# Performance work log

Measured on AMD Instinct MI355X. Metric: run time of the kernel, lower is better.

Reference implementation:

```python
import jax, jax.numpy as jnp
import numpy as np

D_MODEL = 1024
N_HEADS = 16
D_HEAD = D_MODEL // N_HEADS
D_FF = 4096
EPS = 1e-5


def layer_norm(x, g, b):
    mu = jnp.mean(x, axis=-1, keepdims=True)
    var = jnp.mean(jnp.square(x - mu), axis=-1, keepdims=True)
    return (x - mu) * jax.lax.rsqrt(var + EPS) * g + b


def setup_inputs() -> dict:
    key = jax.random.key(0)
    ks = jax.random.split(key, 8)
    s = 1.0 / np.sqrt(D_MODEL)
    return {
        "x": jax.random.normal(ks[0], (2, 2048, D_MODEL), dtype=jnp.float32),
        "Wq": jax.random.normal(ks[1], (N_HEADS, D_MODEL, D_HEAD), dtype=jnp.float32) * s,
        "Wk": jax.random.normal(ks[2], (N_HEADS, D_MODEL, D_HEAD), dtype=jnp.float32) * s,
        "Wv": jax.random.normal(ks[3], (N_HEADS, D_MODEL, D_HEAD), dtype=jnp.float32) * s,
        "Wo": jax.random.normal(ks[4], (D_MODEL, D_MODEL), dtype=jnp.float32) * s,
        "bo": jnp.zeros((D_MODEL,), dtype=jnp.float32),
        "ln1_g": jnp.ones((D_MODEL,), dtype=jnp.float32),
        "ln1_b": jnp.zeros((D_MODEL,), dtype=jnp.float32),
        "ln2_g": jnp.ones((D_MODEL,), dtype=jnp.float32),
        "ln2_b": jnp.zeros((D_MODEL,), dtype=jnp.float32),
        "W1": jax.random.normal(ks[5], (D_MODEL, D_FF), dtype=jnp.float32) * s,
        "b1": jnp.zeros((D_FF,), dtype=jnp.float32),
        "W2": jax.random.normal(ks[6], (D_FF, D_MODEL), dtype=jnp.float32) * (1.0 / np.sqrt(D_FF)),
        "b2": jnp.zeros((D_MODEL,), dtype=jnp.float32),
    }


def reference(x, Wq, Wk, Wv, Wo, bo, ln1_g, ln1_b, ln2_g, ln2_b, W1, b1, W2, b2):
    # Pre-norm MHA (per-head projections batched over head axis h)
    xn = layer_norm(x, ln1_g, ln1_b)
    q = jnp.einsum("bsd,hde->bhse", xn, Wq)
    k = jnp.einsum("bsd,hde->bhse", xn, Wk)
    v = jnp.einsum("bsd,hde->bhse", xn, Wv)
    scores = jnp.einsum("bhqe,bhke->bhqk", q, k) / jnp.sqrt(jnp.float32(D_HEAD))
    w = jax.nn.softmax(scores, axis=-1)
    attn = jnp.einsum("bhqk,bhke->bhqe", w, v)  # [b,h,s,dh]
    b, h, s, dh = attn.shape
    concat = attn.transpose(0, 2, 1, 3).reshape(b, s, h * dh)  # head concat order matches torch cat
    attn_out = concat @ Wo + bo
    hidden = x + attn_out
    hn = layer_norm(hidden, ln2_g, ln2_b)
    ff = jax.nn.gelu(hn @ W1 + b1, approximate=False) @ W2 + b2  # torch nn.GELU default = exact
    return hidden + ff
```

## Files before the change

kernel.cpp:

```cpp
#include <hip/hip_runtime.h>
#include <hip/hip_bf16.h>

typedef __bf16 bf16;
typedef __bf16 bf16x4 __attribute__((ext_vector_type(4)));
typedef __bf16 bf16x8 __attribute__((ext_vector_type(8)));
typedef float  f32x4  __attribute__((ext_vector_type(4)));

static __device__ __forceinline__ f32x4 mfma16(bf16x8 a, bf16x8 b, f32x4 c) {
  return __builtin_amdgcn_mfma_f32_16x16x32_bf16(a, b, c, 0, 0, 0);
}

static __device__ __forceinline__ void gl_lds16(const bf16* g, bf16* l) {
  __builtin_amdgcn_global_load_lds(
      (const __attribute__((address_space(1))) void*)g,
      (__attribute__((address_space(3))) void*)l, 16, 0, 0);
}

struct TrTab {
  const float* src[6];
  bf16* dst[6];
  int R[6], C[6], ntx[6], nty[6];
  int base[7];
};

__global__ __launch_bounds__(256) void tr6_kernel(TrTab tab) {
  int bid = blockIdx.x;
  int j = 0;
  while (j < 5 && bid >= tab.base[j + 1]) ++j;
  const int local = bid - tab.base[j];
  const int R = tab.R[j], C = tab.C[j];
  const int ntx = tab.ntx[j];
  const int per_z = ntx * tab.nty[j];
  const int z = local / per_z;
  const int rem = local - z * per_z;
  const int by = rem / ntx, bx = rem - by * ntx;
  const float* in = tab.src[j];
  bf16* out = tab.dst[j];

  __shared__ bf16 tile[32][33];
  const size_t zoff = (size_t)z * R * C;
  const int tx = threadIdx.x & 31, ty = threadIdx.x >> 5;
  const int x = bx * 32 + tx;
  const int y0 = by * 32;
#pragma unroll
  for (int jj = 0; jj < 4; ++jj)
    tile[ty + jj * 8][tx] = (bf16)in[zoff + (size_t)(y0 + ty + jj * 8) * C + x];
  __syncthreads();
  const int x2 = y0 + tx;
  const int y2 = bx * 32;
#pragma unroll
  for (int jj = 0; jj < 4; ++jj)
    out[zoff + (size_t)(y2 + ty + jj * 8) * R + x2] = tile[tx][ty + jj * 8];
}

__global__ __launch_bounds__(256) void trb_kernel(const bf16* __restrict__ inp,
                                                  bf16* __restrict__ out,
                                                  int R, int C) {
  __shared__ bf16 tile[32][33];
  const size_t zoff = (size_t)blockIdx.z * R * C;
  const int tx = threadIdx.x & 31, ty = threadIdx.x >> 5;
  const int x = blockIdx.x * 32 + tx;
  const int y0 = blockIdx.y * 32;
#pragma unroll
  for (int j = 0; j < 4; ++j)
    tile[ty + j * 8][tx] = inp[zoff + (size_t)(y0 + ty + j * 8) * C + x];
  __syncthreads();
  const int x2 = y0 + tx;
  const int y2 = blockIdx.x * 32;
#pragma unroll
  for (int j = 0; j < 4; ++j)
    out[zoff + (size_t)(y2 + ty + j * 8) * R + x2] = tile[tx][ty + j * 8];
}

__global__ __launch_bounds__(256) void ln_kernel(const float* __restrict__ inp,
                                                 const float* __restrict__ g,
                                                 const float* __restrict__ bt,
                                                 bf16* __restrict__ outp) {
  const int row = blockIdx.x;
  const int t = threadIdx.x;
  f32x4 v = ((const f32x4*)inp)[row * 256 + t];
  float s = v[0] + v[1] + v[2] + v[3];
  float sq = v[0] * v[0] + v[1] * v[1] + v[2] * v[2] + v[3] * v[3];
#pragma unroll
  for (int off = 32; off > 0; off >>= 1) {
    s += __shfl_xor(s, off);
    sq += __shfl_xor(sq, off);
  }
  __shared__ float red[8];
  const int wave = t >> 6, lane = t & 63;
  if (lane == 0) {
    red[wave] = s;
    red[wave + 4] = sq;
  }
  __syncthreads();
  s = red[0] + red[1] + red[2] + red[3];
  sq = red[4] + red[5] + red[6] + red[7];
  const float mu = s * (1.0f / 1024.0f);
  const float var = sq * (1.0f / 1024.0f) - mu * mu;
  const float rstd = rsqrtf(fmaxf(var, 0.0f) + 1e-5f);
  f32x4 gg = ((const f32x4*)g)[t];
  f32x4 bb = ((const f32x4*)bt)[t];
  bf16 o[4];
#pragma unroll
  for (int i = 0; i < 4; ++i)
    o[i] = (bf16)((v[i] - mu) * rstd * gg[i] + bb[i]);
  *(uint2*)&outp[(size_t)row * 1024 + 4 * t] = *(uint2*)o;
}

enum { EPI_QKV = 0, EPI_O = 1, EPI_FF1 = 2, EPI_FF2 = 3 };

template <int EPI, bool NARROW>
__global__ __launch_bounds__(256) void gemm_bt(
    const bf16* __restrict__ A, const bf16* __restrict__ Bt, const int K,
    const float* __restrict__ bias, const float* __restrict__ res,
    bf16* __restrict__ outB, float* __restrict__ outF) {
  constexpr int BN = NARROW ? 64 : 128;
  constexpr int NI = NARROW ? 2 : 4;
  __shared__ __align__(16) bf16 sA[128 * 64];
  __shared__ __align__(16) bf16 sB[BN * 64];
  const int t = threadIdx.x;
  const int lane = t & 63, wave = t >> 6;
  const int quad = lane >> 4, l15 = lane & 15;
  const int wr = wave >> 1, wc = wave & 1;
  const int m0 = blockIdx.y * 128, n0 = blockIdx.x * BN;
  const int srow = lane >> 3;
  const int scol = ((lane & 7) ^ srow) * 8;

  f32x4 acc[4][NI];
#pragma unroll
  for (int i = 0; i < 4; ++i)
#pragma unroll
    for (int j = 0; j < NI; ++j) acc[i][j] = {0.f, 0.f, 0.f, 0.f};

  for (int kt = 0; kt < K; kt += 64) {
    __syncthreads();
#pragma unroll
    for (int c = 0; c < 4; ++c) {
      const int chunk = wave * 4 + c;
      const int row = chunk * 8 + srow;
      gl_lds16(&A[(size_t)(m0 + row) * K + kt + scol], &sA[chunk * 512]);
    }
#pragma unroll
    for (int c = 0; c < BN / 32; ++c) {
      const int chunk = wave * (BN / 32) + c;
      const int row = chunk * 8 + srow;
      gl_lds16(&Bt[(size_t)(n0 + row) * K + kt + scol], &sB[chunk * 512]);
    }
    __syncthreads();
#pragma unroll
    for (int ks = 0; ks < 2; ++ks) {
      bf16x8 af[4], bfr[NI];
#pragma unroll
      for (int mi = 0; mi < 4; ++mi) {
        const int row = wr * 64 + mi * 16 + l15;
        const int col = ((ks * 4 + quad) ^ (row & 7)) * 8;
        af[mi] = *(const bf16x8*)&sA[row * 64 + col];
      }
#pragma unroll
      for (int ni = 0; ni < NI; ++ni) {
        const int row = wc * (BN / 2) + ni * 16 + l15;
        const int col = ((ks * 4 + quad) ^ (row & 7)) * 8;
        bfr[ni] = *(const bf16x8*)&sB[row * 64 + col];
      }
#pragma unroll
      for (int mi = 0; mi < 4; ++mi)
#pragma unroll
        for (int ni = 0; ni < NI; ++ni)
          acc[mi][ni] = mfma16(af[mi], bfr[ni], acc[mi][ni]);
    }
  }

#pragma unroll
  for (int mi = 0; mi < 4; ++mi) {
#pragma unroll
    for (int ni = 0; ni < NI; ++ni) {
      const int n = n0 + wc * (BN / 2) + ni * 16 + l15;
#pragma unroll
      for (int r = 0; r < 4; ++r) {
        const int m = m0 + wr * 64 + mi * 16 + quad * 4 + r;
        float v = acc[mi][ni][r];
        if constexpr (EPI == EPI_QKV) {
          const int which = n >> 10, nn = n & 1023;
          const int h = nn >> 6, e = nn & 63;
          const int b = m >> 11, s2 = m & 2047;
          outB[(size_t)which * 4194304 +
               ((size_t)(b * 16 + h) * 2048 + s2) * 64 + e] = (bf16)v;
        } else if constexpr (EPI == EPI_O) {
          v += bias[n] + res[(size_t)m * 1024 + n];
          outF[(size_t)m * 1024 + n] = v;
        } else if constexpr (EPI == EPI_FF1) {
          v += bias[n];
          v = 0.5f * v * (1.0f + erff(v * 0.70710678118654752f));
          outB[(size_t)m * 4096 + n] = (bf16)v;
        } else {
          v += bias[n] + res[(size_t)m * 1024 + n];
          outF[(size_t)m * 1024 + n] = v;
        }
      }
    }
  }
}

__global__ __launch_bounds__(256) void attn_kernel(const bf16* __restrict__ q,
                                                   const bf16* __restrict__ k,
                                                   const bf16* __restrict__ vt,
                                                   bf16* __restrict__ ao) {
  __shared__ __align__(16) bf16 sQP[64 * 72];
  __shared__ __align__(16) bf16 sK[64 * 64];
  __shared__ __align__(16) bf16 sV[64 * 64];
  const int t = threadIdx.x;
  const int lane = t & 63, wave = t >> 6;
  const int quad = lane >> 4, l15 = lane & 15;
  const int q0 = blockIdx.x * 64;
  const int bh = blockIdx.y;
  const int b = bh >> 4, h = bh & 15;
  const bf16* Q = q + (size_t)bh * 2048 * 64;
  const bf16* Kp = k + (size_t)bh * 2048 * 64;
  const bf16* Vt = vt + (size_t)bh * 64 * 2048;
  const int srow = lane >> 3;
  const int scol = ((lane & 7) ^ srow) * 8;
  const float SCL = 0.125f * 1.4426950408889634f;

#pragma unroll
  for (int c = 0; c < 2; ++c) {
    const int chunk = wave * 2 + c;
    const int row = chunk * 8 + srow;
    gl_lds16(&Q[(size_t)(q0 + row) * 64 + scol], &sQP[chunk * 512]);
  }
  __syncthreads();
  bf16x8 qf[2];
#pragma unroll
  for (int ks = 0; ks < 2; ++ks) {
    const int row = wave * 16 + l15;
    const int col = ((ks * 4 + quad) ^ (row & 7)) * 8;
    qf[ks] = *(const bf16x8*)&sQP[row * 64 + col];
  }

  f32x4 o[4];
  float lsum = 0.f;
#pragma unroll
  for (int ne = 0; ne < 4; ++ne) o[ne] = {0.f, 0.f, 0.f, 0.f};

  for (int kb = 0; kb < 32; ++kb) {
    const int kbase = kb * 64;
    __syncthreads();
#pragma unroll
    for (int c = 0; c < 2; ++c) {
      const int chunk = wave * 2 + c;
      const int row = chunk * 8 + srow;
      gl_lds16(&Kp[(size_t)(kbase + row) * 64 + scol], &sK[chunk * 512]);
      gl_lds16(&Vt[(size_t)row * 2048 + kbase + scol], &sV[chunk * 512]);
    }
    __syncthreads();

    f32x4 s[4];
#pragma unroll
    for (int ni = 0; ni < 4; ++ni) s[ni] = {0.f, 0.f, 0.f, 0.f};
#pragma unroll
    for (int ks = 0; ks < 2; ++ks) {
      bf16x8 kf[4];
#pragma unroll
      for (int ni = 0; ni < 4; ++ni) {
        const int row = ni * 16 + l15;
        const int col = ((ks * 4 + quad) ^ (row & 7)) * 8;
        kf[ni] = *(const bf16x8*)&sK[row * 64 + col];
      }
#pragma unroll
      for (int ni = 0; ni < 4; ++ni)
        s[ni] = mfma16(kf[ni], qf[ks], s[ni]);
    }

#pragma unroll
    for (int ni = 0; ni < 4; ++ni) {
      bf16x4 p4;
#pragma unroll
      for (int r = 0; r < 4; ++r) {
        const float p = exp2f(s[ni][r] * SCL);
        lsum += p;
        p4[r] = (bf16)p;
      }
      *(bf16x4*)&sQP[(wave * 16 + l15) * 72 + ni * 16 + quad * 4] = p4;
    }

#pragma unroll
    for (int ksb = 0; ksb < 2; ++ksb) {
      bf16x8 pf = *(const bf16x8*)&sQP[(wave * 16 + l15) * 72 +
                                       ksb * 32 + quad * 8];
      bf16x8 vf[4];
#pragma unroll
      for (int ne = 0; ne < 4; ++ne) {
        const int row = ne * 16 + l15;
        const int col = ((ksb * 4 + quad) ^ (row & 7)) * 8;
        vf[ne] = *(const bf16x8*)&sV[row * 64 + col];
      }
#pragma unroll
      for (int ne = 0; ne < 4; ++ne)
        o[ne] = mfma16(pf, vf[ne], o[ne]);
    }
  }

  lsum += __shfl_xor(lsum, 16);
  lsum += __shfl_xor(lsum, 32);
  const float linv_q = 1.0f / fmaxf(lsum, 1e-30f);
  float linv[4];
#pragma unroll
  for (int r = 0; r < 4; ++r)
    linv[r] = __shfl(linv_q, quad * 4 + r);
#pragma unroll
  for (int ne = 0; ne < 4; ++ne)
#pragma unroll
    for (int r = 0; r < 4; ++r) {
      const int row = q0 + wave * 16 + quad * 4 + r;
      const int col = h * 64 + ne * 16 + l15;
      ao[((size_t)(b * 2048 + row)) * 1024 + col] =
          (bf16)(o[ne][r] * linv[r]);
    }
}

extern "C" void kernel_launch(void* const* d_in, const int* in_sizes, int n_in,
                              void* d_out, int out_size, void* d_ws,
                              size_t ws_size, hipStream_t stream) {
  const float* x    = (const float*)d_in[0];
  const float* Wq   = (const float*)d_in[1];
  const float* Wk   = (const float*)d_in[2];
  const float* Wv   = (const float*)d_in[3];
  const float* Wo   = (const float*)d_in[4];
  const float* bo   = (const float*)d_in[5];
  const float* ln1g = (const float*)d_in[6];
  const float* ln1b = (const float*)d_in[7];
  const float* ln2g = (const float*)d_in[8];
  const float* ln2b = (const float*)d_in[9];
  const float* W1   = (const float*)d_in[10];
  const float* b1   = (const float*)d_in[11];
  const float* W2   = (const float*)d_in[12];
  const float* b2   = (const float*)d_in[13];

  char* ws = (char*)d_ws;
  const size_t MB = 1ull << 20;
  bf16* QKVT = (bf16*)(ws);
  bf16* WqT  = QKVT;
  bf16* WkT  = (bf16*)(ws + 2 * MB);
  bf16* WvT  = (bf16*)(ws + 4 * MB);
  bf16* WoT  = (bf16*)(ws + 6 * MB);
  bf16* W1T  = (bf16*)(ws + 8 * MB);
  bf16* W2T  = (bf16*)(ws + 16 * MB);
  bf16* sh8  = (bf16*)(ws + 24 * MB);
  bf16* qb   = (bf16*)(ws + 32 * MB);
  bf16* kb   = (bf16*)(ws + 40 * MB);
  bf16* vb   = (bf16*)(ws + 48 * MB);
  bf16* vtb  = (bf16*)(ws + 56 * MB);
  bf16* h1   = (bf16*)(ws + 32 * MB);
  float* hid = (float*)(ws + 64 * MB);

  const dim3 blk(256);

  TrTab tab;
  const float* srcs[6] = {Wq, Wk, Wv, Wo, W1, W2};
  bf16* dsts[6] = {WqT, WkT, WvT, WoT, W1T, W2T};
  const int Rs[6] = {1024, 1024, 1024, 1024, 1024, 4096};
  const int Cs[6] = {64, 64, 64, 1024, 4096, 1024};
  const int Zs[6] = {16, 16, 16, 1, 1, 1};
  int base = 0;
  for (int j = 0; j < 6; ++j) {
    tab.src[j] = srcs[j];
    tab.dst[j] = dsts[j];
    tab.R[j] = Rs[j];
    tab.C[j] = Cs[j];
    tab.ntx[j] = Cs[j] / 32;
    tab.nty[j] = Rs[j] / 32;
    tab.base[j] = base;
    base += (Cs[j] / 32) * (Rs[j] / 32) * Zs[j];
  }
  tab.base[6] = base;
  tr6_kernel<<<base, blk, 0, stream>>>(tab);

  ln_kernel<<<4096, blk, 0, stream>>>(x, ln1g, ln1b, sh8);
  gemm_bt<EPI_QKV, false><<<dim3(24, 32), blk, 0, stream>>>(
      sh8, QKVT, 1024, nullptr, nullptr, qb, nullptr);
  trb_kernel<<<dim3(2, 64, 32), blk, 0, stream>>>(vb, vtb, 2048, 64);
  attn_kernel<<<dim3(32, 32), blk, 0, stream>>>(qb, kb, vtb, sh8);
  gemm_bt<EPI_O, true><<<dim3(16, 32), blk, 0, stream>>>(
      sh8, WoT, 1024, bo, x, nullptr, hid);
  ln_kernel<<<4096, blk, 0, stream>>>(hid, ln2g, ln2b, sh8);
  gemm_bt<EPI_FF1, false><<<dim3(32, 32), blk, 0, stream>>>(
      sh8, W1T, 1024, b1, nullptr, h1, nullptr);
  gemm_bt<EPI_FF2, true><<<dim3(16, 32), blk, 0, stream>>>(
      h1, W2T, 4096, b2, hid, nullptr, (float*)d_out);

  (void)in_sizes; (void)n_in; (void)out_size; (void)ws_size;
}
```

Measured before the change: 378.2 us.

## Split attention keys across two wave groups with 128-query blocks and LDS merge

The attention kernel now uses 512-thread blocks covering 128 queries. Two groups of four waves each process half of the key sequence, and their output accumulators and row sums are merged through LDS at the end. Each wave now handles 32 query rows, so every K/V fragment read from LDS feeds two MFMAs, and the exp2 call switches to the hardware builtin. The cost is twice the register pressure per wave, an extra reduction step through shared memory, and half as many blocks in the grid.

```diff
diff --git a/kernel.cpp b/kernel.cpp
--- a/kernel.cpp
+++ b/kernel.cpp
@@ -8,6 +8,10 @@
 
 static __device__ __forceinline__ f32x4 mfma16(bf16x8 a, bf16x8 b, f32x4 c) {
   return __builtin_amdgcn_mfma_f32_16x16x32_bf16(a, b, c, 0, 0, 0);
+}
+
+static __device__ __forceinline__ float fexp2(float x) {
+  return __builtin_amdgcn_exp2f(x);
 }
 
 static __device__ __forceinline__ void gl_lds16(const bf16* g, bf16* l) {
@@ -201,22 +205,21 @@
   }
 }
 
-__global__ __launch_bounds__(256) void attn_kernel(const bf16* __restrict__ q,
-                                                   const bf16* __restrict__ k,
-                                                   const bf16* __restrict__ vt,
-                                                   bf16* __restrict__ ao) {
-  __shared__ __align__(16) bf16 sQP[64 * 72];
-  __shared__ __align__(16) bf16 sK[64 * 64];
-  __shared__ __align__(16) bf16 sV[64 * 64];
+__global__ __launch_bounds__(512, 4) void attn_kernel(
+    const bf16* __restrict__ q, const bf16* __restrict__ k,
+    const bf16* __restrict__ vt, bf16* __restrict__ ao) {
+  __shared__ __align__(16) bf16 sP[256 * 72];
+  __shared__ __align__(16) bf16 sK[2][64 * 64];
+  __shared__ __align__(16) bf16 sV[2][64 * 64];
   const int t = threadIdx.x;
   const int lane = t & 63, wave = t >> 6;
+  const int wq = wave & 3, kh = wave >> 2;
   const int quad = lane >> 4, l15 = lane & 15;
-  const int q0 = blockIdx.x * 64;
-  const int bh = blockIdx.y;
-  const int b = bh >> 4, h = bh & 15;
-  const bf16* Q = q + (size_t)bh * 2048 * 64;
-  const bf16* Kp = k + (size_t)bh * 2048 * 64;
-  const bf16* Vt = vt + (size_t)bh * 64 * 2048;
+  const int q0 = blockIdx.x * 128;
+  const int bh = blockIdx.y, b = bh >> 4, h = bh & 15;
+  const bf16* Q  = q  + (size_t)bh * 2048 * 64;
+  const bf16* Kp = k  + (size_t)bh * 2048 * 64 + (size_t)kh * 1024 * 64;
+  const bf16* Vt = vt + (size_t)bh * 64 * 2048 + kh * 1024;
   const int srow = lane >> 3;
   const int scol = ((lane & 7) ^ srow) * 8;
   const float SCL = 0.125f * 1.4426950408889634f;
@@ -225,37 +228,44 @@
   for (int c = 0; c < 2; ++c) {
     const int chunk = wave * 2 + c;
     const int row = chunk * 8 + srow;
-    gl_lds16(&Q[(size_t)(q0 + row) * 64 + scol], &sQP[chunk * 512]);
-  }
-  __syncthreads();
-  bf16x8 qf[2];
-#pragma unroll
-  for (int ks = 0; ks < 2; ++ks) {
-    const int row = wave * 16 + l15;
-    const int col = ((ks * 4 + quad) ^ (row & 7)) * 8;
-    qf[ks] = *(const bf16x8*)&sQP[row * 64 + col];
-  }
-
-  f32x4 o[4];
-  float lsum = 0.f;
-#pragma unroll
-  for (int ne = 0; ne < 4; ++ne) o[ne] = {0.f, 0.f, 0.f, 0.f};
-
-  for (int kb = 0; kb < 32; ++kb) {
+    gl_lds16(&Q[(size_t)(q0 + row) * 64 + scol], &sP[chunk * 512]);
+  }
+  __syncthreads();
+  bf16x8 qf[2][2];
+#pragma unroll
+  for (int mi = 0; mi < 2; ++mi)
+#pragma unroll
+    for (int ks = 0; ks < 2; ++ks) {
+      const int row = wq * 32 + mi * 16 + l15;
+      const int col = ((ks * 4 + quad) ^ (row & 7)) * 8;
+      qf[mi][ks] = *(const bf16x8*)&sP[row * 64 + col];
+    }
+  __syncthreads();
+
+  f32x4 o[2][4];
+  float ls[2] = {0.f, 0.f};
+#pragma unroll
+  for (int mi = 0; mi < 2; ++mi)
+#pragma unroll
+    for (int ne = 0; ne < 4; ++ne) o[mi][ne] = {0.f, 0.f, 0.f, 0.f};
+
+  for (int kb = 0; kb < 16; ++kb) {
     const int kbase = kb * 64;
     __syncthreads();
 #pragma unroll
     for (int c = 0; c < 2; ++c) {
-      const int chunk = wave * 2 + c;
+      const int chunk = wq * 2 + c;
       const int row = chunk * 8 + srow;
-      gl_lds16(&Kp[(size_t)(kbase + row) * 64 + scol], &sK[chunk * 512]);
-      gl_lds16(&Vt[(size_t)row * 2048 + kbase + scol], &sV[chunk * 512]);
+      gl_lds16(&Kp[(size_t)(kbase + row) * 64 + scol], &sK[kh][chunk * 512]);
+      gl_lds16(&Vt[(size_t)row * 2048 + kbase + scol], &sV[kh][chunk * 512]);
     }
     __syncthreads();
 
-    f32x4 s[4];
-#pragma unroll
-    for (int ni = 0; ni < 4; ++ni) s[ni] = {0.f, 0.f, 0.f, 0.f};
+    f32x4 s[4][2];
+#pragma unroll
+    for (int ni = 0; ni < 4; ++ni)
+#pragma unroll
+      for (int mi = 0; mi < 2; ++mi) s[ni][mi] = {0.f, 0.f, 0.f, 0.f};
 #pragma unroll
     for (int ks = 0; ks < 2; ++ks) {
       bf16x8 kf[4];
@@ -263,58 +273,99 @@
       for (int ni = 0; ni < 4; ++ni) {
         const int row = ni * 16 + l15;
         const int col = ((ks * 4 + quad) ^ (row & 7)) * 8;
-        kf[ni] = *(const bf16x8*)&sK[row * 64 + col];
+        kf[ni] = *(const bf16x8*)&sK[kh][row * 64 + col];
       }
 #pragma unroll
       for (int ni = 0; ni < 4; ++ni)
-        s[ni] = mfma16(kf[ni], qf[ks], s[ni]);
-    }
-
-#pragma unroll
-    for (int ni = 0; ni < 4; ++ni) {
-      bf16x4 p4;
-#pragma unroll
-      for (int r = 0; r < 4; ++r) {
-        const float p = exp2f(s[ni][r] * SCL);
-        lsum += p;
-        p4[r] = (bf16)p;
-      }
-      *(bf16x4*)&sQP[(wave * 16 + l15) * 72 + ni * 16 + quad * 4] = p4;
-    }
+#pragma unroll
+        for (int mi = 0; mi < 2; ++mi)
+          s[ni][mi] = mfma16(kf[ni], qf[mi][ks], s[ni][mi]);
+    }
+
+#pragma unroll
+    for (int mi = 0; mi < 2; ++mi)
+#pragma unroll
+      for (int ni = 0; ni < 4; ++ni) {
+        bf16x4 p4;
+#pragma unroll
+        for (int r = 0; r < 4; ++r) {
+          const float p = fexp2(s[ni][mi][r] * SCL);
+          ls[mi] += p;
+          p4[r] = (bf16)p;
+        }
+        *(bf16x4*)&sP[(wave * 32 + mi * 16 + l15) * 72 + ni * 16 + quad * 4] =
+            p4;
+      }
 
 #pragma unroll
     for (int ksb = 0; ksb < 2; ++ksb) {
-      bf16x8 pf = *(const bf16x8*)&sQP[(wave * 16 + l15) * 72 +
-                                       ksb * 32 + quad * 8];
       bf16x8 vf[4];
 #pragma unroll
       for (int ne = 0; ne < 4; ++ne) {
         const int row = ne * 16 + l15;
         const int col = ((ksb * 4 + quad) ^ (row & 7)) * 8;
-        vf[ne] = *(const bf16x8*)&sV[row * 64 + col];
-      }
+        vf[ne] = *(const bf16x8*)&sV[kh][row * 64 + col];
+      }
+#pragma unroll
+      for (int mi = 0; mi < 2; ++mi) {
+        const bf16x8 pf = *(const bf16x8*)&sP[(wave * 32 + mi * 16 + l15) * 72 +
+                                              ksb * 32 + quad * 8];
+#pragma unroll
+        for (int ne = 0; ne < 4; ++ne)
+          o[mi][ne] = mfma16(pf, vf[ne], o[mi][ne]);
+      }
+    }
+  }
+
+#pragma unroll
+  for (int mi = 0; mi < 2; ++mi) {
+    ls[mi] += __shfl_xor(ls[mi], 16);
+    ls[mi] += __shfl_xor(ls[mi], 32);
+  }
+
+  float* mo = (float*)sP;
+  float* ml = (float*)sK;
+  __syncthreads();
+  if (kh == 1) {
+    const int base = (wq * 64 + lane) * 32;
+#pragma unroll
+    for (int mi = 0; mi < 2; ++mi)
 #pragma unroll
       for (int ne = 0; ne < 4; ++ne)
-        o[ne] = mfma16(pf, vf[ne], o[ne]);
-    }
-  }
-
-  lsum += __shfl_xor(lsum, 16);
-  lsum += __shfl_xor(lsum, 32);
-  const float linv_q = 1.0f / fmaxf(lsum, 1e-30f);
-  float linv[4];
-#pragma unroll
-  for (int r = 0; r < 4; ++r)
-    linv[r] = __shfl(linv_q, quad * 4 + r);
-#pragma unroll
-  for (int ne = 0; ne < 4; ++ne)
-#pragma unroll
-    for (int r = 0; r < 4; ++r) {
-      const int row = q0 + wave * 16 + quad * 4 + r;
-      const int col = h * 64 + ne * 16 + l15;
-      ao[((size_t)(b * 2048 + row)) * 1024 + col] =
-          (bf16)(o[ne][r] * linv[r]);
-    }
+        *(f32x4*)&mo[base + (mi * 4 + ne) * 4] = o[mi][ne];
+    ml[(wq * 64 + lane) * 2 + 0] = ls[0];
+    ml[(wq * 64 + lane) * 2 + 1] = ls[1];
+  }
+  __syncthreads();
+  if (kh == 0) {
+    const int base = (wq * 64 + lane) * 32;
+#pragma unroll
+    for (int mi = 0; mi < 2; ++mi) {
+#pragma unroll
+      for (int ne = 0; ne < 4; ++ne) {
+        const f32x4 add = *(const f32x4*)&mo[base + (mi * 4 + ne) * 4];
+#pragma unroll
+        for (int r = 0; r < 4; ++r) o[mi][ne][r] += add[r];
+      }
+      ls[mi] += ml[(wq * 64 + lane) * 2 + mi];
+      ls[mi] = 1.0f / fmaxf(ls[mi], 1e-30f);
+    }
+#pragma unroll
+    for (int mi = 0; mi < 2; ++mi) {
+      float linv[4];
+#pragma unroll
+      for (int r = 0; r < 4; ++r) linv[r] = __shfl(ls[mi], quad * 4 + r);
+#pragma unroll
+      for (int ne = 0; ne < 4; ++ne)
+#pragma unroll
+        for (int r = 0; r < 4; ++r) {
+          const int row = q0 + wq * 32 + mi * 16 + quad * 4 + r;
+          const int col = h * 64 + ne * 16 + l15;
+          ao[((size_t)(b * 2048 + row)) * 1024 + col] =
+              (bf16)(o[mi][ne][r] * linv[r]);
+        }
+    }
+  }
 }
 
 extern "C" void kernel_launch(void* const* d_in, const int* in_sizes, int n_in,
@@ -378,7 +429,7 @@
   gemm_bt<EPI_QKV, false><<<dim3(24, 32), blk, 0, stream>>>(
       sh8, QKVT, 1024, nullptr, nullptr, qb, nullptr);
   trb_kernel<<<dim3(2, 64, 32), blk, 0, stream>>>(vb, vtb, 2048, 64);
-  attn_kernel<<<dim3(32, 32), blk, 0, stream>>>(qb, kb, vtb, sh8);
+  attn_kernel<<<dim3(16, 32), dim3(512), 0, stream>>>(qb, kb, vtb, sh8);
   gemm_bt<EPI_O, true><<<dim3(16, 32), blk, 0, stream>>>(
       sh8, WoT, 1024, bo, x, nullptr, hid);
   ln_kernel<<<4096, blk, 0, stream>>>(hid, ln2g, ln2b, sh8);
```

Result: no change. 373.8 us (-1.1%).
